# Kernel tuning notes

Hardware: AMD Instinct MI355X
Metric: run time of the kernel (lower is better)

Reference implementation:

```python
import jax, jax.numpy as jnp
import numpy as np
import math

B, T, C = 4, 2048, 1024
N_HEAD = 16
HEAD = C // N_HEAD  # 64
ROPE_BASE = 10000.0


def rotate_half(x):
    x1, x2 = x[..., : x.shape[-1] // 2], x[..., x.shape[-1] // 2:]
    return jnp.concatenate((-x2, x1), axis=-1)


def rope_cos_sin(seq_len, dim, dtype=jnp.float32):
    inv_freq = 1.0 / (ROPE_BASE ** (jnp.arange(0, dim, 2, dtype=jnp.float32) / dim))
    t = jnp.arange(seq_len, dtype=jnp.float32)
    freqs = jnp.einsum('i,j->ij', t, inv_freq)          # [T, dim/2]
    emb = jnp.concatenate((freqs, freqs), axis=-1)       # [T, dim]
    return jnp.cos(emb).astype(dtype), jnp.sin(emb).astype(dtype)


def setup_inputs() -> dict:
    key = jax.random.key(0)
    ks = jax.random.split(key, 5)
    s_in = 1.0 / math.sqrt(C)
    return {
        'x': jax.random.normal(ks[0], (B, T, C), dtype=jnp.float32),
        'W_qkv': jax.random.normal(ks[1], (C, 3 * C), dtype=jnp.float32) * s_in,
        'b_qkv': jnp.zeros((3 * C,), dtype=jnp.float32),
        'W_proj': jax.random.normal(ks[2], (C, C), dtype=jnp.float32) * s_in,
        'b_proj': jnp.zeros((C,), dtype=jnp.float32),
    }


def reference(x, W_qkv, b_qkv, W_proj, b_proj):
    b, t, c = x.shape
    qkv = x @ W_qkv + b_qkv                               # [B,T,3C]
    q, k, v = jnp.split(qkv, 3, axis=-1)
    # [B,T,C] -> [B,H,T,hd]
    def to_heads(u):
        return u.reshape(b, t, N_HEAD, HEAD).transpose(0, 2, 1, 3)
    q, k, v = to_heads(q), to_heads(k), to_heads(v)
    # RoPE
    cos, sin = rope_cos_sin(t, HEAD, x.dtype)             # [T,hd]
    cos = cos[None, None]; sin = sin[None, None]
    q = q * cos + rotate_half(q) * sin
    k = k * cos + rotate_half(k) * sin
    # naive causal attention (materializes [B,H,T,T] like the original)
    att = jnp.einsum('bhqd,bhkd->bhqk', q, k) * (1.0 / math.sqrt(HEAD))
    causal = jnp.tril(jnp.ones((t, t), dtype=bool))
    att = jnp.where(causal[None, None], att, -jnp.inf)
    att = jax.nn.softmax(att, axis=-1)
    y = jnp.einsum('bhqk,bhkd->bhqd', att, v)             # [B,H,T,hd]
    y = y.transpose(0, 2, 1, 3).reshape(b, t, c)
    return y @ W_proj + b_proj
```

## Files before the change

### kernel.cpp

```cpp
#include <hip/hip_runtime.h>
#include <stdint.h>

#define B_  4
#define T_  2048
#define C_  1024
#define NH_ 16
#define HD_ 64
#define BH_ (B_*NH_)
#define M_  (B_*T_)

using f32x4  = __attribute__((ext_vector_type(4))) float;
using f32x16 = __attribute__((ext_vector_type(16))) float;
using bf16x8 = __attribute__((ext_vector_type(8))) short;

__device__ __forceinline__ unsigned short f2bf(float x) {
  union { float f; uint32_t u; } v; v.f = x;
  uint32_t u = v.u;
  return (unsigned short)((u + 0x7FFFu + ((u >> 16) & 1u)) >> 16);
}

__device__ __forceinline__ uint32_t cvtpk(float a, float b) {
  uint32_t r;
  asm("v_cvt_pk_bf16_f32 %0, %1, %2" : "=v"(r) : "v"(a), "v"(b));
  return r;
}

__device__ __forceinline__ void gload16(const void* g, void* l) {
  __builtin_amdgcn_global_load_lds(
      (const __attribute__((address_space(1))) void*)g,
      (__attribute__((address_space(3))) void*)l, 16, 0, 0);
}

#define BAR() do { asm volatile("" ::: "memory"); __builtin_amdgcn_s_barrier(); \
                   asm volatile("" ::: "memory"); } while (0)
#define VMC(N) asm volatile("s_waitcnt vmcnt(" #N ")" ::: "memory")


__global__ void k_cvt_bf16(const float* __restrict__ src,
                           unsigned short* __restrict__ dst, int n) {
  int i = (blockIdx.x * 256 + threadIdx.x) * 4;
  if (i + 3 < n) {
    float4 v = *(const float4*)(src + i);
    ushort4 o;
    o.x = f2bf(v.x); o.y = f2bf(v.y); o.z = f2bf(v.z); o.w = f2bf(v.w);
    *(ushort4*)(dst + i) = o;
  }
}

__global__ void k_transpose_w(const float* __restrict__ W,
                              unsigned short* __restrict__ WT, int K, int N) {
  __shared__ float tile[32][33];
  int bx = blockIdx.x, by = blockIdx.y;
  int tx = threadIdx.x, ty = threadIdx.y;
  #pragma unroll
  for (int i = 0; i < 32; i += 8)
    tile[ty + i][tx] = W[(size_t)(by*32 + ty + i) * N + bx*32 + tx];
  __syncthreads();
  #pragma unroll
  for (int i = 0; i < 32; i += 8)
    WT[(size_t)(bx*32 + ty + i) * K + by*32 + tx] = f2bf(tile[tx][ty + i]);
}

__global__ void k_rope_tab(float* __restrict__ cosT, float* __restrict__ sinT) {
  int t = blockIdx.x * 8 + threadIdx.y;
  int i = threadIdx.x;
  float inv = expf(-(float)i * (9.210340371976184f / 32.0f));
  float f = (float)t * inv;
  cosT[t*32 + i] = cosf(f);
  sinT[t*32 + i] = sinf(f);
}

template<int N, int K, int EPI>
__global__ __launch_bounds__(256)
void k_gemm(const unsigned short* __restrict__ Ag,
            const unsigned short* __restrict__ BT,
            const float* __restrict__ bias,
            const float* __restrict__ cosT,
            const float* __restrict__ sinT,
            unsigned short* __restrict__ Qh,
            unsigned short* __restrict__ Kh,
            unsigned short* __restrict__ VhT,
            float* __restrict__ outF) {
  __shared__ alignas(16) unsigned short As[2][128*64];
  __shared__ alignas(16) unsigned short Bs[2][128*64];
  const int tid  = threadIdx.x;
  const int lane = tid & 63;
  const int wv   = tid >> 6;
  const int wm   = wv >> 1, wn = wv & 1;
  const int l15  = lane & 15, l4 = lane >> 4;
  const int NT  = N / 128;
  const int id  = ((int)blockIdx.x & 7) * ((int)gridDim.x >> 3) + ((int)blockIdx.x >> 3);
  const int m0  = (id / NT) * 128;
  const int n0  = (id % NT) * 128;

  f32x4 acc[4][4] = {};

  auto stage = [&](int buf, int kt) {
    #pragma unroll
    for (int it = 0; it < 4; ++it) {
      int idx  = it*256 + wv*64 + lane;
      int row  = idx >> 3, slot = idx & 7;
      int g    = slot ^ (row & 7);
      gload16(Ag + (size_t)(m0 + row) * K + kt*64 + g*8,
              (void*)(As[buf] + (it*256 + wv*64) * 8));
      gload16(BT + (size_t)(n0 + row) * K + kt*64 + g*8,
              (void*)(Bs[buf] + (it*256 + wv*64) * 8));
    }
  };

  stage(0, 0);
  int cur = 0;

  for (int kt = 0; kt < K/64; ++kt) {
    if (kt + 1 < K/64) {
      stage(cur ^ 1, kt + 1);
      VMC(8);
    } else {
      VMC(0);
    }
    BAR();
    #pragma unroll
    for (int ks = 0; ks < 2; ++ks) {
      bf16x8 af[4], bfr[4];
      #pragma unroll
      for (int mi = 0; mi < 4; ++mi) {
        int r = wm*64 + mi*16 + l15;
        int g = (ks*4 + l4) ^ (r & 7);
        af[mi] = *(const bf16x8*)(As[cur] + r*64 + g*8);
      }
      #pragma unroll
      for (int ni = 0; ni < 4; ++ni) {
        int r = wn*64 + ni*16 + l15;
        int g = (ks*4 + l4) ^ (r & 7);
        bfr[ni] = *(const bf16x8*)(Bs[cur] + r*64 + g*8);
      }
      __builtin_amdgcn_s_setprio(1);
      #pragma unroll
      for (int mi = 0; mi < 4; ++mi)
        #pragma unroll
        for (int ni = 0; ni < 4; ++ni)
          acc[mi][ni] = __builtin_amdgcn_mfma_f32_16x16x32_bf16(
              af[mi], bfr[ni], acc[mi][ni], 0, 0, 0);
      __builtin_amdgcn_s_setprio(0);
    }
    BAR();
    cur ^= 1;
  }

  if (EPI == 0) {
    const int ncol = n0 + wn*64;
    const int part = ncol >> 10;
    const int hid  = (ncol & 1023) >> 6;
    unsigned short* dstQK = (part == 0) ? Qh : Kh;
    #pragma unroll
    for (int mi = 0; mi < 4; ++mi) {
      #pragma unroll
      for (int j = 0; j < 4; ++j) {
        int row = m0 + wm*64 + mi*16 + l4*4 + j;
        int bb = row >> 11, tt = row & 2047;
        if (part < 2) {
          size_t base = ((size_t)((bb*NH_ + hid) * T_ + tt)) * HD_;
          #pragma unroll
          for (int ni = 0; ni < 2; ++ni) {
            int d = ni*16 + l15;
            float a1 = acc[mi][ni][j]     + bias[ncol + d];
            float a2 = acc[mi][ni + 2][j] + bias[ncol + d + 32];
            float cv = cosT[tt*32 + d], sv = sinT[tt*32 + d];
            float o1 = a1*cv - a2*sv;
            float o2 = a2*cv + a1*sv;
            if (part == 0) { o1 *= 0.18033688011112042f; o2 *= 0.18033688011112042f; }
            dstQK[base + d]      = f2bf(o1);
            dstQK[base + d + 32] = f2bf(o2);
          }
        } else {
          #pragma unroll
          for (int ni = 0; ni < 4; ++ni) {
            int d = ni*16 + l15;
            float av = acc[mi][ni][j] + bias[ncol + d];
            VhT[((size_t)((bb*NH_ + hid) * HD_ + d)) * T_ + tt] = f2bf(av);
          }
        }
      }
    }
  } else {
    #pragma unroll
    for (int mi = 0; mi < 4; ++mi)
      #pragma unroll
      for (int ni = 0; ni < 4; ++ni)
        #pragma unroll
        for (int j = 0; j < 4; ++j) {
          int row = m0 + wm*64 + mi*16 + l4*4 + j;
          int col = n0 + wn*64 + ni*16 + l15;
          outF[(size_t)row * N + col] = acc[mi][ni][j] + bias[col];
        }
  }
}

__global__ __launch_bounds__(256, 3)
void k_attn(const unsigned short* __restrict__ Qh,
            const unsigned short* __restrict__ Kh,
            const unsigned short* __restrict__ VhT,
            unsigned short* __restrict__ Y) {
  __shared__ alignas(16) unsigned short Ks[2][64*64];
  __shared__ alignas(16) unsigned short Vs[2][64*64];
  const int tid  = threadIdx.x;
  const int lane = tid & 63;
  const int wv   = tid >> 6;
  const int l31  = lane & 31;
  const int h    = lane >> 5;
  const int bh   = blockIdx.x & 63;
  const int qb   = 15 - (blockIdx.x >> 6);
  const int r32  = qb*128 + wv*32;
  const int nt   = 2*qb + 2;
  const int qg   = r32 + l31;

  bf16x8 qf[4];
  #pragma unroll
  for (int i = 0; i < 4; ++i)
    qf[i] = *(const bf16x8*)(Qh + ((size_t)(bh*T_ + qg))*HD_ + i*16 + h*8);

  float m_r = -1e30f, l_r = 0.f;
  f32x16 o[2] = {};

  auto stage = [&](int buf, int jt) {
    #pragma unroll
    for (int it = 0; it < 2; ++it) {
      int idx = it*256 + wv*64 + lane;
      int row = idx >> 3, slot = idx & 7;
      int g   = slot ^ (row & 7);
      gload16(Kh  + ((size_t)(bh*T_ + jt*64 + row))*HD_ + g*8,
              (void*)(Ks[buf] + (it*256 + wv*64)*8));
      gload16(VhT + ((size_t)(bh*HD_ + row))*T_ + jt*64 + g*8,
              (void*)(Vs[buf] + (it*256 + wv*64)*8));
    }
  };

  stage(0, 0);
  int cur = 0;

  for (int jt = 0; jt < nt; ++jt) {
    if (jt + 1 < nt) {
      stage(cur ^ 1, jt + 1);
      VMC(4);
    } else {
      VMC(0);
    }
    BAR();

    if (jt*64 <= r32 + 31) {
      f32x16 s[2] = {f32x16{0}, f32x16{0}};
      __builtin_amdgcn_s_setprio(1);
      #pragma unroll
      for (int kb = 0; kb < 2; ++kb)
        #pragma unroll
        for (int i = 0; i < 4; ++i) {
          int r = kb*32 + l31;
          int g = (2*i + h) ^ (r & 7);
          bf16x8 kf = *(const bf16x8*)(Ks[cur] + r*64 + g*8);
          s[kb] = __builtin_amdgcn_mfma_f32_32x32x16_bf16(kf, qf[i], s[kb], 0, 0, 0);
        }
      __builtin_amdgcn_s_setprio(0);

      float p[2][16];
      const bool diag = (jt + 1)*64 > r32;
      #pragma unroll
      for (int kb = 0; kb < 2; ++kb)
        #pragma unroll
        for (int r = 0; r < 16; ++r) {
          float v = s[kb][r];
          if (diag) {
            int key = jt*64 + kb*32 + (r & 3) + 8*(r >> 2) + 4*h;
            v = (key > qg) ? -1e30f : v;
          }
          p[kb][r] = v;
        }

      float mx[16];
      #pragma unroll
      for (int r = 0; r < 16; ++r) mx[r] = fmaxf(p[0][r], p[1][r]);
      #pragma unroll
      for (int st = 8; st > 0; st >>= 1)
        #pragma unroll
        for (int r = 0; r < 8; ++r)
          if (r < st) mx[r] = fmaxf(mx[r], mx[r + st]);
      float tm = fmaxf(mx[0], __shfl_xor(mx[0], 32));

      if (!__all(tm <= m_r + 8.0f)) {
        float mn = fmaxf(m_r, tm);
        float scale = exp2f(m_r - mn);
        m_r = mn;
        l_r *= scale;
        #pragma unroll
        for (int dblk = 0; dblk < 2; ++dblk)
          #pragma unroll
          for (int r = 0; r < 16; ++r)
            o[dblk][r] *= scale;
      }

      #pragma unroll
      for (int kb = 0; kb < 2; ++kb)
        #pragma unroll
        for (int r = 0; r < 16; ++r)
          p[kb][r] = exp2f(p[kb][r] - m_r);

      float sm[16];
      #pragma unroll
      for (int r = 0; r < 16; ++r) sm[r] = p[0][r] + p[1][r];
      #pragma unroll
      for (int st = 8; st > 0; st >>= 1)
        #pragma unroll
        for (int r = 0; r < 8; ++r)
          if (r < st) sm[r] += sm[r + st];
      l_r += sm[0] + __shfl_xor(sm[0], 32);

      #pragma unroll
      for (int kb = 0; kb < 2; ++kb) {
        uint32_t a01 = cvtpk(p[kb][0],  p[kb][1]);
        uint32_t a23 = cvtpk(p[kb][2],  p[kb][3]);
        uint32_t a45 = cvtpk(p[kb][4],  p[kb][5]);
        uint32_t a67 = cvtpk(p[kb][6],  p[kb][7]);
        uint32_t b01 = cvtpk(p[kb][8],  p[kb][9]);
        uint32_t b23 = cvtpk(p[kb][10], p[kb][11]);
        uint32_t b45 = cvtpk(p[kb][12], p[kb][13]);
        uint32_t b67 = cvtpk(p[kb][14], p[kb][15]);
        uint32_t s1 = h ? a01 : a45, s2 = h ? a23 : a67;
        uint32_t s3 = h ? b01 : b45, s4 = h ? b23 : b67;
        uint32_t x1 = __shfl_xor(s1, 32), x2 = __shfl_xor(s2, 32);
        uint32_t x3 = __shfl_xor(s3, 32), x4 = __shfl_xor(s4, 32);
        union { bf16x8 v; uint32_t d[4]; } f0, f1;
        f0.d[0] = h ? x1 : a01;  f0.d[1] = h ? x2 : a23;
        f0.d[2] = h ? a45 : x1;  f0.d[3] = h ? a67 : x2;
        f1.d[0] = h ? x3 : b01;  f1.d[1] = h ? x4 : b23;
        f1.d[2] = h ? b45 : x3;  f1.d[3] = h ? b67 : x4;

        __builtin_amdgcn_s_setprio(1);
        #pragma unroll
        for (int koff = 0; koff < 2; ++koff) {
          bf16x8 pf = koff ? f1.v : f0.v;
          #pragma unroll
          for (int dblk = 0; dblk < 2; ++dblk) {
            int rv = dblk*32 + l31;
            int gv = (kb*4 + koff*2 + h) ^ (rv & 7);
            bf16x8 vf = *(const bf16x8*)(Vs[cur] + rv*64 + gv*8);
            o[dblk] = __builtin_amdgcn_mfma_f32_32x32x16_bf16(vf, pf, o[dblk], 0, 0, 0);
          }
        }
        __builtin_amdgcn_s_setprio(0);
      }
    }

    BAR();
    cur ^= 1;
  }

  int b = bh >> 4, hd = bh & 15;
  float rinv = 1.0f / l_r;
  unsigned short* yrow = Y + ((size_t)(b*T_ + r32 + l31))*C_ + hd*64;
  #pragma unroll
  for (int dblk = 0; dblk < 2; ++dblk)
    #pragma unroll
    for (int g2 = 0; g2 < 4; ++g2) {
      ushort4 o4;
      o4.x = f2bf(o[dblk][g2*4 + 0] * rinv);
      o4.y = f2bf(o[dblk][g2*4 + 1] * rinv);
      o4.z = f2bf(o[dblk][g2*4 + 2] * rinv);
      o4.w = f2bf(o[dblk][g2*4 + 3] * rinv);
      *(ushort4*)(yrow + dblk*32 + g2*8 + 4*h) = o4;
    }
}


extern "C" void kernel_launch(void* const* d_in, const int* in_sizes, int n_in,
                              void* d_out, int out_size, void* d_ws, size_t ws_size,
                              hipStream_t stream) {
  const float* x      = (const float*)d_in[0];
  const float* W_qkv  = (const float*)d_in[1];
  const float* b_qkv  = (const float*)d_in[2];
  const float* W_proj = (const float*)d_in[3];
  const float* b_proj = (const float*)d_in[4];
  float* out = (float*)d_out;

  char* ws = (char*)d_ws;
  size_t off = 0;
  auto alloc = [&](size_t bytes) {
    void* p = ws + off; off += (bytes + 255) & ~(size_t)255; return p;
  };
  unsigned short* xb     = (unsigned short*)alloc((size_t)M_ * C_ * 2);
  unsigned short* WqkvT  = (unsigned short*)alloc((size_t)3 * C_ * C_ * 2);
  unsigned short* WprojT = (unsigned short*)alloc((size_t)C_ * C_ * 2);
  unsigned short* Qh     = (unsigned short*)alloc((size_t)M_ * C_ * 2);
  unsigned short* Kh     = (unsigned short*)alloc((size_t)M_ * C_ * 2);
  unsigned short* VhT    = (unsigned short*)alloc((size_t)M_ * C_ * 2);
  float* cosT = (float*)alloc((size_t)T_ * 32 * 4);
  float* sinT = (float*)alloc((size_t)T_ * 32 * 4);
  unsigned short* Y = xb;

  k_cvt_bf16<<<(M_*C_/4 + 255)/256, 256, 0, stream>>>(x, xb, M_*C_);
  dim3 tb(32, 8);
  k_transpose_w<<<dim3(3*C_/32, C_/32), tb, 0, stream>>>(W_qkv, WqkvT, C_, 3*C_);
  k_transpose_w<<<dim3(C_/32,   C_/32), tb, 0, stream>>>(W_proj, WprojT, C_, C_);
  k_rope_tab<<<T_/8, tb, 0, stream>>>(cosT, sinT);

  k_gemm<3*C_, C_, 0><<<dim3(1536), 256, 0, stream>>>(
      xb, WqkvT, b_qkv, cosT, sinT, Qh, Kh, VhT, nullptr);

  k_attn<<<dim3(T_/128 * BH_), 256, 0, stream>>>(Qh, Kh, VhT, Y);

  k_gemm<C_, C_, 1><<<dim3(512), 256, 0, stream>>>(
      Y, WprojT, b_proj, nullptr, nullptr, nullptr, nullptr, nullptr, out);
}
```

Baseline: 211.7 us.

## Enlarge GEMM tile to 128x256, single-buffer LDS, each wave owns a 64-column slab

The bf16 GEMM kernels move from 128x128 tiles with a 2x2 wave grid and double-buffered LDS to 128x256 tiles where each of four waves computes all 128 rows against its own 64 columns. LDS goes from double buffering to a single buffer, with a barrier before each stage and a full vmcnt(0) wait. Address computation is hoisted into precomputed pointers and launch bounds now request 2 blocks per CU. The aim is more reuse per LDS byte and fewer blocks, at the cost of losing load/compute overlap, doubling accumulator registers, and halving the grid for the 1024-wide projection (256 blocks).

```diff
diff --git a/kernel.cpp b/kernel.cpp
--- a/kernel.cpp
+++ b/kernel.cpp
@@ -71,7 +71,7 @@
 }
 
 template<int N, int K, int EPI>
-__global__ __launch_bounds__(256)
+__global__ __launch_bounds__(256, 2)
 void k_gemm(const unsigned short* __restrict__ Ag,
             const unsigned short* __restrict__ BT,
             const float* __restrict__ bias,
@@ -81,82 +81,78 @@
             unsigned short* __restrict__ Kh,
             unsigned short* __restrict__ VhT,
             float* __restrict__ outF) {
-  __shared__ alignas(16) unsigned short As[2][128*64];
-  __shared__ alignas(16) unsigned short Bs[2][128*64];
+  __shared__ alignas(16) unsigned short As[128*64];
+  __shared__ alignas(16) unsigned short Bs[256*64];
   const int tid  = threadIdx.x;
   const int lane = tid & 63;
   const int wv   = tid >> 6;
-  const int wm   = wv >> 1, wn = wv & 1;
   const int l15  = lane & 15, l4 = lane >> 4;
-  const int NT  = N / 128;
+  const int NT  = N / 256;
   const int id  = ((int)blockIdx.x & 7) * ((int)gridDim.x >> 3) + ((int)blockIdx.x >> 3);
   const int m0  = (id / NT) * 128;
-  const int n0  = (id % NT) * 128;
-
-  f32x4 acc[4][4] = {};
-
-  auto stage = [&](int buf, int kt) {
-    #pragma unroll
-    for (int it = 0; it < 4; ++it) {
-      int idx  = it*256 + wv*64 + lane;
-      int row  = idx >> 3, slot = idx & 7;
-      int g    = slot ^ (row & 7);
-      gload16(Ag + (size_t)(m0 + row) * K + kt*64 + g*8,
-              (void*)(As[buf] + (it*256 + wv*64) * 8));
-      gload16(BT + (size_t)(n0 + row) * K + kt*64 + g*8,
-              (void*)(Bs[buf] + (it*256 + wv*64) * 8));
-    }
-  };
-
-  stage(0, 0);
-  int cur = 0;
-
+  const int n0  = (id % NT) * 256;
+
+  f32x4 acc[8][4] = {};
+
+  const int g0 = l4 ^ (l15 & 7);
+  const int g1 = (4 + l4) ^ (l15 & 7);
+  const unsigned short* aK0 = &As[l15*64 + g0*8];
+  const unsigned short* aK1 = &As[l15*64 + g1*8];
+  const unsigned short* bK0 = &Bs[(wv*64 + l15)*64 + g0*8];
+  const unsigned short* bK1 = &Bs[(wv*64 + l15)*64 + g1*8];
+
+  const int srow = tid >> 3;
+  const int sg   = (tid & 7) ^ (srow & 7);
+  const int voff = srow*K + sg*8;
+  const int ldsD = wv*512;
+  const unsigned short* Abase = Ag + (size_t)m0*K;
+  const unsigned short* Bbase = BT + (size_t)n0*K;
+
+#define STG(KT) do { \
+  const int _u = (KT)*64; \
+  _Pragma("unroll") for (int c = 0; c < 4; ++c) \
+    gload16(Abase + (c*(32*K) + _u) + voff, (void*)(&As[c*2048 + ldsD])); \
+  _Pragma("unroll") for (int c = 0; c < 8; ++c) \
+    gload16(Bbase + (c*(32*K) + _u) + voff, (void*)(&Bs[c*2048 + ldsD])); \
+} while (0)
+
+  #pragma unroll 1
   for (int kt = 0; kt < K/64; ++kt) {
-    if (kt + 1 < K/64) {
-      stage(cur ^ 1, kt + 1);
-      VMC(8);
-    } else {
-      VMC(0);
-    }
+    if (kt) BAR();
+    STG(kt);
+    VMC(0);
     BAR();
     #pragma unroll
     for (int ks = 0; ks < 2; ++ks) {
-      bf16x8 af[4], bfr[4];
-      #pragma unroll
-      for (int mi = 0; mi < 4; ++mi) {
-        int r = wm*64 + mi*16 + l15;
-        int g = (ks*4 + l4) ^ (r & 7);
-        af[mi] = *(const bf16x8*)(As[cur] + r*64 + g*8);
-      }
-      #pragma unroll
-      for (int ni = 0; ni < 4; ++ni) {
-        int r = wn*64 + ni*16 + l15;
-        int g = (ks*4 + l4) ^ (r & 7);
-        bfr[ni] = *(const bf16x8*)(Bs[cur] + r*64 + g*8);
-      }
+      const unsigned short* ar = ks ? aK1 : aK0;
+      const unsigned short* br = ks ? bK1 : bK0;
+      bf16x8 bfr[4], afr[8];
+      #pragma unroll
+      for (int ni = 0; ni < 4; ++ni) bfr[ni] = *(const bf16x8*)(br + ni*1024);
+      #pragma unroll
+      for (int mi = 0; mi < 8; ++mi) afr[mi] = *(const bf16x8*)(ar + mi*1024);
       __builtin_amdgcn_s_setprio(1);
       #pragma unroll
-      for (int mi = 0; mi < 4; ++mi)
+      for (int mi = 0; mi < 8; ++mi)
         #pragma unroll
         for (int ni = 0; ni < 4; ++ni)
           acc[mi][ni] = __builtin_amdgcn_mfma_f32_16x16x32_bf16(
-              af[mi], bfr[ni], acc[mi][ni], 0, 0, 0);
+              afr[mi], bfr[ni], acc[mi][ni], 0, 0, 0);
       __builtin_amdgcn_s_setprio(0);
     }
-    BAR();
-    cur ^= 1;
   }
+#undef STG
 
   if (EPI == 0) {
-    const int ncol = n0 + wn*64;
+    const int ncol = n0 + wv*64;
     const int part = ncol >> 10;
     const int hid  = (ncol & 1023) >> 6;
     unsigned short* dstQK = (part == 0) ? Qh : Kh;
     #pragma unroll
-    for (int mi = 0; mi < 4; ++mi) {
+    for (int mi = 0; mi < 8; ++mi) {
       #pragma unroll
       for (int j = 0; j < 4; ++j) {
-        int row = m0 + wm*64 + mi*16 + l4*4 + j;
+        int row = m0 + mi*16 + l4*4 + j;
         int bb = row >> 11, tt = row & 2047;
         if (part < 2) {
           size_t base = ((size_t)((bb*NH_ + hid) * T_ + tt)) * HD_;
@@ -184,13 +180,13 @@
     }
   } else {
     #pragma unroll
-    for (int mi = 0; mi < 4; ++mi)
+    for (int mi = 0; mi < 8; ++mi)
       #pragma unroll
       for (int ni = 0; ni < 4; ++ni)
         #pragma unroll
         for (int j = 0; j < 4; ++j) {
-          int row = m0 + wm*64 + mi*16 + l4*4 + j;
-          int col = n0 + wn*64 + ni*16 + l15;
+          int row = m0 + mi*16 + l4*4 + j;
+          int col = n0 + wv*64 + ni*16 + l15;
           outF[(size_t)row * N + col] = acc[mi][ni][j] + bias[col];
         }
   }
@@ -401,11 +397,11 @@
   k_transpose_w<<<dim3(C_/32,   C_/32), tb, 0, stream>>>(W_proj, WprojT, C_, C_);
   k_rope_tab<<<T_/8, tb, 0, stream>>>(cosT, sinT);
 
-  k_gemm<3*C_, C_, 0><<<dim3(1536), 256, 0, stream>>>(
+  k_gemm<3*C_, C_, 0><<<dim3(768), 256, 0, stream>>>(
       xb, WqkvT, b_qkv, cosT, sinT, Qh, Kh, VhT, nullptr);
 
   k_attn<<<dim3(T_/128 * BH_), 256, 0, stream>>>(Qh, Kh, VhT, Y);
 
-  k_gemm<C_, C_, 1><<<dim3(512), 256, 0, stream>>>(
+  k_gemm<C_, C_, 1><<<dim3(256), 256, 0, stream>>>(
       Y, WprojT, b_proj, nullptr, nullptr, nullptr, nullptr, nullptr, out);
 }
```

After: 217.0 us. 2.5% more time.
